# Optimization experiments

Measured on AMD Instinct MI355X. Metric: run time of the kernel, lower is better.

Reference implementation:

```python
import jax, jax.numpy as jnp
import numpy as np

B, V, H = 16384, 1024, 256


def setup_inputs() -> dict:
    key = jax.random.key(0)
    k1, k2 = jax.random.split(key)
    # binary spin configurations in {0,1}
    batch = jax.random.bernoulli(k1, 0.5, (B, V)).astype(jnp.float32)
    # small weights + negative hidden bias keep exp(log p*) finite in fp32
    weights_amp = jax.random.normal(k2, (H, V), dtype=jnp.float32) * (0.05 / np.sqrt(V))
    visible_bias_amp = jnp.zeros((V,), dtype=jnp.float32)
    hidden_bias_amp = -5.0 * jnp.ones((H,), dtype=jnp.float32)
    return {
        'batch': batch,
        'weights_amp': weights_amp,
        'visible_bias_amp': visible_bias_amp,
        'hidden_bias_amp': hidden_bias_amp,
        'k': 8,
    }


def _gibbs_sampling_amp(v0, W, vb, hb, k, key):
    """k steps of block Gibbs sampling, vectorized over the whole batch [B,V]."""
    keys = jax.random.split(key, 2 * k).reshape(k, 2)

    def step(v, ks):
        ph = jax.nn.sigmoid(v @ W.T + hb)                      # [B,H]
        h = (jax.random.uniform(ks[0], ph.shape) < ph).astype(v.dtype)
        pv = jax.nn.sigmoid(h @ W + vb)                        # [B,V]
        v = (jax.random.uniform(ks[1], pv.shape) < pv).astype(v.dtype)
        return v, None

    vk, _ = jax.lax.scan(step, v0, keys)
    return vk


def reference(batch, weights_amp, visible_bias_amp, hidden_bias_amp, k):
    W, vb, hb = weights_amp, visible_bias_amp, hidden_bias_amp
    nbatch = batch.shape[0]
    key = jax.random.key(42)

    vk = _gibbs_sampling_amp(batch, W, vb, hb, k, key)          # [B,V]

    ph0 = jax.nn.sigmoid(batch @ W.T + hb)                      # [B,H] positive-phase hidden probs
    pre_k = vk @ W.T + hb                                       # [B,H]
    phk = jax.nn.sigmoid(pre_k)                                 # [B,H] negative-phase hidden probs

    # unnormalized_probability_amp(vk) = exp(vk.vb + sum_j softplus((W vk + hb)_j))
    log_p = vk @ vb + jax.nn.softplus(pre_k).sum(axis=-1)       # [B]
    inv_norm = jnp.exp(-log_p) / nbatch                         # 1 / (len(batch) * p*(vk))

    # g_W = sum_b [outer(phk_b, vk_b) - outer(ph0_b, v0_b)] / norm_b
    g_w = (jnp.einsum('b,bh,bv->hv', inv_norm, phk, vk)
           - jnp.einsum('b,bh,bv->hv', inv_norm, ph0, batch))   # [H,V]
    g_vb = jnp.einsum('b,bv->v', inv_norm, vk - batch)          # [V]
    g_hb = jnp.einsum('b,bh->h', inv_norm, phk - ph0)           # [H]

    return jnp.concatenate([g_w.ravel(), g_vb, g_hb])
```

## Files before the change

### kernel.cpp

```cpp
#include <hip/hip_runtime.h>
#include <stdint.h>

#define B_DIM 16384
#define V_DIM 1024
#define H_DIM 256
#define K_STEPS 8

typedef short bf16x8 __attribute__((ext_vector_type(8)));
typedef float f32x4 __attribute__((ext_vector_type(4)));

__host__ __device__ inline uint32_t rotl32(uint32_t v, int r) {
#if defined(__HIP_DEVICE_COMPILE__)
    return __builtin_amdgcn_alignbit(v, v, (uint32_t)(32 - r));
#else
    return (v << r) | (v >> (32 - r));
#endif
}

__host__ __device__ inline void threefry2x32(uint32_t k0, uint32_t k1,
                                             uint32_t x0, uint32_t x1,
                                             uint32_t* o0, uint32_t* o1) {
    uint32_t k2 = k0 ^ k1 ^ 0x1BD11BDAu;
    x0 += k0; x1 += k1;
#define TF_RND(r) { x0 += x1; x1 = rotl32(x1, (r)); x1 ^= x0; }
    TF_RND(13) TF_RND(15) TF_RND(26) TF_RND(6)
    x0 += k1; x1 += k2 + 1u;
    TF_RND(17) TF_RND(29) TF_RND(16) TF_RND(24)
    x0 += k2; x1 += k0 + 2u;
    TF_RND(13) TF_RND(15) TF_RND(26) TF_RND(6)
    x0 += k0; x1 += k1 + 3u;
    TF_RND(17) TF_RND(29) TF_RND(16) TF_RND(24)
    x0 += k1; x1 += k2 + 4u;
    TF_RND(13) TF_RND(15) TF_RND(26) TF_RND(6)
    x0 += k2; x1 += k0 + 5u;
#undef TF_RND
    *o0 = x0; *o1 = x1;
}

__device__ inline float tf_uniform(uint32_t key0, uint32_t key1, uint32_t e) {
    uint32_t o0, o1;
    threefry2x32(key0, key1, 0u, e, &o0, &o1);
    uint32_t bits = o0 ^ o1;
    return __uint_as_float((bits >> 9) | 0x3f800000u) - 1.0f;
}

__device__ inline uint16_t bf16_rn(float f) {
    uint32_t u = __float_as_uint(f);
    uint32_t r = u + 0x7FFFu + ((u >> 16) & 1u);
    return (uint16_t)(r >> 16);
}
__device__ inline float bf16_to_f32(uint16_t h) {
    return __uint_as_float(((uint32_t)h) << 16);
}

__device__ inline void gload_lds16(const void* g, void* l) {
    __builtin_amdgcn_global_load_lds((const __attribute__((address_space(1))) uint32_t*)g,
                                     (__attribute__((address_space(3))) uint32_t*)l, 16, 0, 0);
}

template <int MODE>
__global__ __launch_bounds__(256, 4) void mfma_gemm(
    const ushort* __restrict__ A, const ushort* __restrict__ Bhi,
    const ushort* __restrict__ Blo, const float* __restrict__ bias,
    ushort* __restrict__ out, ushort* __restrict__ out2,
    int N, int K, uint32_t key0, uint32_t key1) {
    __shared__ __align__(16) ushort As[2][64 * 32];
    __shared__ __align__(16) ushort Bs[2][64 * 32];
    __shared__ __align__(16) ushort Bs2[2][64 * 32];

    const int tid = threadIdx.x;
    const int lane = tid & 63;
    const int w = tid >> 6;
    const int m0 = blockIdx.x * 64;
    const int n0 = blockIdx.y * 64;

    f32x4 acc[2][2] = {};

    const int wm = (w & 1) * 32;
    const int wn = (w >> 1) * 32;
    const int q = lane >> 4;
    const int l15 = lane & 15;
    const int srow = lane >> 2;
    const int scol = (lane & 3) * 8;

    const size_t arow = (size_t)(m0 + w * 16 + srow) * K;
    const size_t brow = (size_t)(n0 + w * 16 + srow) * K;

    for (int k0 = 0; k0 < K; k0 += 64) {
#pragma unroll
        for (int s = 0; s < 2; ++s) {
            gload_lds16(&A[arow + k0 + s * 32 + scol], &As[s][w * 512]);
            gload_lds16(&Bhi[brow + k0 + s * 32 + scol], &Bs[s][w * 512]);
            gload_lds16(&Blo[brow + k0 + s * 32 + scol], &Bs2[s][w * 512]);
        }
        __syncthreads();
#pragma unroll
        for (int s = 0; s < 2; ++s) {
            bf16x8 af[2], bh[2], bl[2];
#pragma unroll
            for (int i = 0; i < 2; ++i)
                af[i] = *(const bf16x8*)&As[s][(wm + i * 16 + l15) * 32 + q * 8];
#pragma unroll
            for (int j = 0; j < 2; ++j) {
                bh[j] = *(const bf16x8*)&Bs[s][(wn + j * 16 + l15) * 32 + q * 8];
                bl[j] = *(const bf16x8*)&Bs2[s][(wn + j * 16 + l15) * 32 + q * 8];
            }
#pragma unroll
            for (int i = 0; i < 2; ++i)
#pragma unroll
                for (int j = 0; j < 2; ++j) {
                    acc[i][j] = __builtin_amdgcn_mfma_f32_16x16x32_bf16(af[i], bh[j], acc[i][j], 0, 0, 0);
                    acc[i][j] = __builtin_amdgcn_mfma_f32_16x16x32_bf16(af[i], bl[j], acc[i][j], 0, 0, 0);
                }
        }
        __syncthreads();
    }

    const int orow = q * 4;
#pragma unroll
    for (int i = 0; i < 2; ++i) {
#pragma unroll
        for (int j = 0; j < 2; ++j) {
            int col = n0 + wn + j * 16 + l15;
            float bv = bias[col];
#pragma unroll
            for (int r = 0; r < 4; ++r) {
                int row = m0 + wm + i * 16 + orow + r;
                float val = acc[i][j][r] + bv;
                if (MODE == 0) {
                    float E = expf(-val);
                    uint32_t e = (uint32_t)row * (uint32_t)N + (uint32_t)col;
                    float u = tf_uniform(key0, key1, e);
                    out[(size_t)row * N + col] = (fmaf(u, E, u) < 1.0f) ? (ushort)0x3F80 : (ushort)0;
                } else if (MODE == 3) {
                    float E = expf(-val);
                    float sg = 1.0f / (1.0f + E);
                    uint32_t e = (uint32_t)row * (uint32_t)N + (uint32_t)col;
                    float u = tf_uniform(key0, key1, e);
                    out[(size_t)row * N + col] = (fmaf(u, E, u) < 1.0f) ? (ushort)0x3F80 : (ushort)0;
                    out2[(size_t)row * N + col] = bf16_rn(sg);
                } else {
                    float sg = 1.0f / (1.0f + expf(-val));
                    out[(size_t)row * N + col] = bf16_rn(sg);
                }
            }
        }
    }
}

__global__ __launch_bounds__(256, 8) void vsample_kernel(
    const ushort* __restrict__ h,
    const float* __restrict__ W,
    const float* __restrict__ vb,
    ushort* __restrict__ vout,
    uint32_t key0, uint32_t key1) {
    const int lane = threadIdx.x & 63;
    const int wid = threadIdx.x >> 6;

    float vbr[16];
#pragma unroll
    for (int t = 0; t < 16; ++t) vbr[t] = vb[lane + 64 * t];

    const int row_base = blockIdx.x * 8 + wid * 2;
#pragma unroll
    for (int rr = 0; rr < 2; ++rr) {
        const int b = row_base + rr;
        ushort4 hv = ((const ushort4*)(h + (size_t)b * H_DIM))[lane];
        unsigned long long masks[4];
        masks[0] = __ballot(hv.x != 0);
        masks[1] = __ballot(hv.y != 0);
        masks[2] = __ballot(hv.z != 0);
        masks[3] = __ballot(hv.w != 0);

        float acc[16];
#pragma unroll
        for (int t = 0; t < 16; ++t) acc[t] = 0.0f;

#pragma unroll
        for (int s = 0; s < 4; ++s) {
            unsigned long long m = masks[s];
            while (m) {
                int l = __ffsll(m) - 1;
                m &= m - 1;
                int j = l * 4 + s;
                const float* wrow = W + (size_t)j * V_DIM + lane;
#pragma unroll
                for (int t = 0; t < 16; ++t) acc[t] += wrow[64 * t];
            }
        }

        const uint32_t ebase = (uint32_t)b * (uint32_t)V_DIM + (uint32_t)lane;
        ushort* orow = vout + (size_t)b * V_DIM + lane;
#pragma unroll
        for (int t = 0; t < 16; ++t) {
            float pre = acc[t] + vbr[t];
            float E = expf(-pre);
            float u = tf_uniform(key0, key1, ebase + 64u * (uint32_t)t);
            orow[64 * t] = (fmaf(u, E, u) < 1.0f) ? (ushort)0x3F80 : (ushort)0;
        }
    }
}

__global__ __launch_bounds__(256, 4) void mfma_gemm_acc(
    const ushort* __restrict__ A, const ushort* __restrict__ Bt,
    float* __restrict__ out, int N, int K, int k_slice) {
    __shared__ __align__(16) ushort As[64 * 32];
    __shared__ __align__(16) ushort Bs[64 * 32];

    const int tid = threadIdx.x;
    const int lane = tid & 63;
    const int w = tid >> 6;
    const int m0 = blockIdx.x * 64;
    const int n0 = blockIdx.y * 64;
    const int kbase = blockIdx.z * k_slice;

    f32x4 acc[2][2] = {};

    const int wm = (w & 1) * 32;
    const int wn = (w >> 1) * 32;
    const int q = lane >> 4;
    const int l15 = lane & 15;
    const int srow = lane >> 2;
    const int scol = (lane & 3) * 8;

    const size_t arow = (size_t)(m0 + w * 16 + srow) * K;
    const size_t brow = (size_t)(n0 + w * 16 + srow) * K;

    for (int kt = 0; kt < k_slice; kt += 32) {
        const int k0 = kbase + kt;
        gload_lds16(&A[arow + k0 + scol], &As[w * 512]);
        gload_lds16(&Bt[brow + k0 + scol], &Bs[w * 512]);
        __syncthreads();
        bf16x8 af[2], bf[2];
#pragma unroll
        for (int i = 0; i < 2; ++i) {
            af[i] = *(const bf16x8*)&As[(wm + i * 16 + l15) * 32 + q * 8];
            bf[i] = *(const bf16x8*)&Bs[(wn + i * 16 + l15) * 32 + q * 8];
        }
#pragma unroll
        for (int i = 0; i < 2; ++i)
#pragma unroll
            for (int j = 0; j < 2; ++j)
                acc[i][j] = __builtin_amdgcn_mfma_f32_16x16x32_bf16(af[i], bf[j], acc[i][j], 0, 0, 0);
        __syncthreads();
    }

    const int orow = q * 4;
#pragma unroll
    for (int i = 0; i < 2; ++i)
#pragma unroll
        for (int j = 0; j < 2; ++j) {
            int col = n0 + wn + j * 16 + l15;
#pragma unroll
            for (int r = 0; r < 4; ++r) {
                int row = m0 + wm + i * 16 + orow + r;
                atomicAdd(&out[(size_t)row * N + col], acc[i][j][r]);
            }
        }
}

__global__ void wsplit_kernel(const float* __restrict__ W, ushort* __restrict__ whi,
                              ushort* __restrict__ wlo) {
    int idx = blockIdx.x * 256 + threadIdx.x;
    float w = W[idx];
    ushort hi = bf16_rn(w);
    float fhi = bf16_to_f32(hi);
    ushort lo = bf16_rn(w - fhi);
    whi[idx] = hi; wlo[idx] = lo;
}

__global__ void tobf16_kernel(const float* __restrict__ src, ushort* __restrict__ dst) {
    int idx = blockIdx.x * 256 + threadIdx.x;
    float4 f = ((const float4*)src)[idx];
    ushort4 o;
    o.x = bf16_rn(f.x); o.y = bf16_rn(f.y); o.z = bf16_rn(f.z); o.w = bf16_rn(f.w);
    ((ushort4*)dst)[idx] = o;
}

__global__ __launch_bounds__(256) void lognorm_kernel(
    const ushort* __restrict__ phk, const ushort* __restrict__ vk,
    const float* __restrict__ vb, float* __restrict__ inv) {
    int b = blockIdx.x;
    int tid = threadIdx.x;
    float p = bf16_to_f32(phk[(size_t)b * H_DIM + tid]);
    float s = -log1pf(-p);
    for (int j = tid; j < V_DIM; j += 256)
        s += bf16_to_f32(vk[(size_t)b * V_DIM + j]) * vb[j];
    for (int off = 32; off > 0; off >>= 1) s += __shfl_down(s, off, 64);
    __shared__ float wsum[4];
    int lane = tid & 63, wid = tid >> 6;
    if (lane == 0) wsum[wid] = s;
    __syncthreads();
    if (tid == 0) {
        float t = wsum[0] + wsum[1] + wsum[2] + wsum[3];
        inv[b] = expf(-t) * (1.0f / 16384.0f);
    }
}

__global__ void build_At(const ushort* __restrict__ P, const float* __restrict__ inv,
                         float sgn, ushort* __restrict__ At) {
    __shared__ float T[64][65];
    int c = threadIdx.x & 63;
    int rb = threadIdx.x >> 6;
    int b0 = blockIdx.x * 64;
    int h0 = blockIdx.y * 64;
    for (int r = rb; r < 64; r += 4) {
        int b = b0 + r;
        T[c][r] = sgn * inv[b] * bf16_to_f32(P[(size_t)b * H_DIM + h0 + c]);
    }
    __syncthreads();
    for (int r = rb; r < 64; r += 4)
        At[(size_t)(h0 + r) * B_DIM + b0 + c] = bf16_rn(T[r][c]);
}

__global__ void build_Bt(const ushort* __restrict__ Sb, const float* __restrict__ Sf,
                         int use_f32, ushort* __restrict__ Bt) {
    __shared__ ushort T[64][65];
    int c = threadIdx.x & 63;
    int rb = threadIdx.x >> 6;
    int b0 = blockIdx.x * 64;
    int v0 = blockIdx.y * 64;
    for (int r = rb; r < 64; r += 4) {
        int b = b0 + r;
        T[c][r] = use_f32 ? bf16_rn(Sf[(size_t)b * V_DIM + v0 + c])
                          : Sb[(size_t)b * V_DIM + v0 + c];
    }
    __syncthreads();
    for (int r = rb; r < 64; r += 4)
        Bt[(size_t)(v0 + r) * B_DIM + b0 + c] = T[r][c];
}

__global__ void gvb_kernel(const ushort* __restrict__ vk, const ushort* __restrict__ vbat,
                           const float* __restrict__ inv, float* __restrict__ gvb) {
    int col = blockIdx.x * 256 + threadIdx.x;
    int b0 = blockIdx.y * 512;
    float acc = 0.0f;
    for (int r = 0; r < 512; ++r) {
        int b = b0 + r;
        acc += inv[b] * (bf16_to_f32(vk[(size_t)b * V_DIM + col]) -
                         bf16_to_f32(vbat[(size_t)b * V_DIM + col]));
    }
    atomicAdd(&gvb[col], acc);
}

__global__ void ghb_kernel(const ushort* __restrict__ phk, const ushort* __restrict__ ph0,
                           const float* __restrict__ inv, float* __restrict__ ghb) {
    int col = threadIdx.x;
    int b0 = blockIdx.x * 256;
    float acc = 0.0f;
    for (int r = 0; r < 256; ++r) {
        int b = b0 + r;
        acc += inv[b] * (bf16_to_f32(phk[(size_t)b * H_DIM + col]) -
                         bf16_to_f32(ph0[(size_t)b * H_DIM + col]));
    }
    atomicAdd(&ghb[col], acc);
}

extern "C" void kernel_launch(void* const* d_in, const int* in_sizes, int n_in,
                              void* d_out, int out_size, void* d_ws, size_t ws_size,
                              hipStream_t stream) {
    const float* batch = (const float*)d_in[0];
    const float* W = (const float*)d_in[1];
    const float* vb = (const float*)d_in[2];
    const float* hb = (const float*)d_in[3];

    char* base = (char*)d_ws;
    ushort* w_hi  = (ushort*)(base + 0);
    ushort* w_lo  = (ushort*)(base + 524288);
    ushort* v_cur = (ushort*)(base + 2097152);
    float*  inv   = (float*)(base + 35651584);
    ushort* h_cur = (ushort*)(base + 35717120);
    ushort* At    = h_cur;
    ushort* batch_bf = (ushort*)(base + 44105728);
    ushort* Bt    = batch_bf;
    ushort* ph0b  = (ushort*)(base + 77660160);
    ushort* phkb  = (ushort*)(base + 86048768);

    float* gw  = (float*)d_out;
    float* gvb = gw + (size_t)H_DIM * V_DIM;
    float* ghb = gvb + V_DIM;

    hipMemsetAsync(d_out, 0, (size_t)out_size * sizeof(float), stream);

    uint32_t sk0[16], sk1[16];
    for (int n = 0; n < 16; ++n) threefry2x32(0u, 42u, 0u, (uint32_t)n, &sk0[n], &sk1[n]);

    wsplit_kernel<<<dim3(1024), dim3(256), 0, stream>>>(W, w_hi, w_lo);
    tobf16_kernel<<<dim3(B_DIM * V_DIM / 4 / 256), dim3(256), 0, stream>>>(batch, batch_bf);

    for (int i = 0; i < K_STEPS; ++i) {
        const ushort* vin = (i == 0) ? batch_bf : v_cur;
        if (i == 0) {
            mfma_gemm<3><<<dim3(B_DIM / 64, H_DIM / 64), dim3(256), 0, stream>>>(
                vin, w_hi, w_lo, hb, h_cur, ph0b, H_DIM, V_DIM, sk0[0], sk1[0]);
        } else {
            mfma_gemm<0><<<dim3(B_DIM / 64, H_DIM / 64), dim3(256), 0, stream>>>(
                vin, w_hi, w_lo, hb, h_cur, nullptr, H_DIM, V_DIM, sk0[2 * i], sk1[2 * i]);
        }
        vsample_kernel<<<dim3(B_DIM / 8), dim3(256), 0, stream>>>(
            h_cur, W, vb, v_cur, sk0[2 * i + 1], sk1[2 * i + 1]);
    }
    mfma_gemm<1><<<dim3(B_DIM / 64, H_DIM / 64), dim3(256), 0, stream>>>(
        v_cur, w_hi, w_lo, hb, phkb, nullptr, H_DIM, V_DIM, 0u, 0u);

    lognorm_kernel<<<dim3(B_DIM), dim3(256), 0, stream>>>(phkb, v_cur, vb, inv);
    ghb_kernel<<<dim3(B_DIM / 256), dim3(256), 0, stream>>>(phkb, ph0b, inv, ghb);
    gvb_kernel<<<dim3(V_DIM / 256, B_DIM / 512), dim3(256), 0, stream>>>(v_cur, batch_bf, inv, gvb);

    build_At<<<dim3(B_DIM / 64, H_DIM / 64), dim3(256), 0, stream>>>(phkb, inv, 1.0f, At);
    build_Bt<<<dim3(B_DIM / 64, V_DIM / 64), dim3(256), 0, stream>>>(v_cur, nullptr, 0, Bt);
    mfma_gemm_acc<<<dim3(H_DIM / 64, V_DIM / 64, 16), dim3(256), 0, stream>>>(
        At, Bt, gw, V_DIM, B_DIM, 1024);
    build_At<<<dim3(B_DIM / 64, H_DIM / 64), dim3(256), 0, stream>>>(ph0b, inv, -1.0f, At);
    build_Bt<<<dim3(B_DIM / 64, V_DIM / 64), dim3(256), 0, stream>>>(nullptr, batch, 1, Bt);
    mfma_gemm_acc<<<dim3(H_DIM / 64, V_DIM / 64, 16), dim3(256), 0, stream>>>(
        At, Bt, gw, V_DIM, B_DIM, 1024);
}
```

Before: 901.2 us.

## Fuse all Gibbs steps into one persistent per-row-tile kernel with LDS hidden state

Replaces the 17 separate launches of the hidden GEMM and visible sampling kernels with a single kernel. Each 512-thread block owns 32 batch rows and iterates all Gibbs steps plus the final phk computation. The sampled hidden units stay in LDS instead of round-tripping through global memory, and launch overhead between steps goes away. In exchange, each block streams the full 256-row split weight matrix every step, the grid shrinks to 512 blocks with a larger LDS footprint per block, and the GEMM tile becomes 32x256, which may reduce occupancy and latency hiding.

```diff
diff --git a/kernel.cpp b/kernel.cpp
--- a/kernel.cpp
+++ b/kernel.cpp
@@ -58,146 +58,143 @@
                                      (__attribute__((address_space(3))) uint32_t*)l, 16, 0, 0);
 }
 
-template <int MODE>
-__global__ __launch_bounds__(256, 4) void mfma_gemm(
-    const ushort* __restrict__ A, const ushort* __restrict__ Bhi,
-    const ushort* __restrict__ Blo, const float* __restrict__ bias,
-    ushort* __restrict__ out, ushort* __restrict__ out2,
-    int N, int K, uint32_t key0, uint32_t key1) {
-    __shared__ __align__(16) ushort As[2][64 * 32];
-    __shared__ __align__(16) ushort Bs[2][64 * 32];
-    __shared__ __align__(16) ushort Bs2[2][64 * 32];
+struct KeyPack { uint32_t hk0[8], hk1[8], vk0[8], vk1[8]; };
+
+__global__ __launch_bounds__(512, 4) void gibbs_fused(
+    const ushort* __restrict__ batch_bf,
+    const ushort* __restrict__ Whi, const ushort* __restrict__ Wlo,
+    const float* __restrict__ Wf, const float* __restrict__ vb,
+    const float* __restrict__ hb, ushort* __restrict__ v_cur,
+    ushort* __restrict__ ph0b, ushort* __restrict__ phkb, KeyPack kp) {
+    __shared__ __align__(16) ushort As[2][32 * 32];
+    __shared__ __align__(16) ushort BhS[2][256 * 32];
+    __shared__ __align__(16) ushort BlS[2][256 * 32];
 
     const int tid = threadIdx.x;
     const int lane = tid & 63;
     const int w = tid >> 6;
-    const int m0 = blockIdx.x * 64;
-    const int n0 = blockIdx.y * 64;
-
-    f32x4 acc[2][2] = {};
-
-    const int wm = (w & 1) * 32;
-    const int wn = (w >> 1) * 32;
+    const int m0 = blockIdx.x * 32;
+
+    const int wm = (w & 1) * 16;
+    const int wn = (w >> 1) * 64;
     const int q = lane >> 4;
     const int l15 = lane & 15;
     const int srow = lane >> 2;
     const int scol = (lane & 3) * 8;
 
-    const size_t arow = (size_t)(m0 + w * 16 + srow) * K;
-    const size_t brow = (size_t)(n0 + w * 16 + srow) * K;
-
-    for (int k0 = 0; k0 < K; k0 += 64) {
-#pragma unroll
-        for (int s = 0; s < 2; ++s) {
-            gload_lds16(&A[arow + k0 + s * 32 + scol], &As[s][w * 512]);
-            gload_lds16(&Bhi[brow + k0 + s * 32 + scol], &Bs[s][w * 512]);
-            gload_lds16(&Blo[brow + k0 + s * 32 + scol], &Bs2[s][w * 512]);
+    ushort* h_lds = &BhS[0][0];
+
+    for (int step = 0; step <= K_STEPS; ++step) {
+        const ushort* Asrc = (step == 0) ? batch_bf : v_cur;
+        f32x4 acc[4] = {};
+
+        for (int k0 = 0; k0 < V_DIM; k0 += 64) {
+            if (w < 4) {
+                const int s = w & 1, rh = w >> 1;
+                gload_lds16(&Asrc[(size_t)(m0 + rh * 16 + srow) * V_DIM + k0 + s * 32 + scol],
+                            &As[s][rh * 512]);
+            }
+#pragma unroll
+            for (int c = 0; c < 4; ++c) {
+                const int cc = w + 8 * c;
+                const int s = cc & 1, rb = cc >> 1;
+                const size_t off = (size_t)(rb * 16 + srow) * V_DIM + k0 + s * 32 + scol;
+                gload_lds16(&Whi[off], &BhS[s][rb * 512]);
+                gload_lds16(&Wlo[off], &BlS[s][rb * 512]);
+            }
+            __syncthreads();
+#pragma unroll
+            for (int s = 0; s < 2; ++s) {
+                bf16x8 af = *(const bf16x8*)&As[s][(wm + l15) * 32 + q * 8];
+#pragma unroll
+                for (int j = 0; j < 4; ++j) {
+                    bf16x8 bh = *(const bf16x8*)&BhS[s][(wn + j * 16 + l15) * 32 + q * 8];
+                    bf16x8 bl = *(const bf16x8*)&BlS[s][(wn + j * 16 + l15) * 32 + q * 8];
+                    acc[j] = __builtin_amdgcn_mfma_f32_16x16x32_bf16(af, bh, acc[j], 0, 0, 0);
+                    acc[j] = __builtin_amdgcn_mfma_f32_16x16x32_bf16(af, bl, acc[j], 0, 0, 0);
+                }
+            }
+            __syncthreads();
+        }
+
+        if (step == K_STEPS) {
+#pragma unroll
+            for (int j = 0; j < 4; ++j) {
+                const int col = wn + j * 16 + l15;
+                const float hbv = hb[col];
+#pragma unroll
+                for (int r = 0; r < 4; ++r) {
+                    const int row = m0 + wm + q * 4 + r;
+                    float val = acc[j][r] + hbv;
+                    phkb[(size_t)row * H_DIM + col] = bf16_rn(1.0f / (1.0f + expf(-val)));
+                }
+            }
+            break;
+        }
+
+        const uint32_t kh0 = kp.hk0[step], kh1 = kp.hk1[step];
+#pragma unroll
+        for (int j = 0; j < 4; ++j) {
+            const int col = wn + j * 16 + l15;
+            const float hbv = hb[col];
+#pragma unroll
+            for (int r = 0; r < 4; ++r) {
+                const int rowl = wm + q * 4 + r;
+                const int row = m0 + rowl;
+                float val = acc[j][r] + hbv;
+                float E = expf(-val);
+                float u = tf_uniform(kh0, kh1, (uint32_t)row * (uint32_t)H_DIM + (uint32_t)col);
+                h_lds[rowl * H_DIM + col] = (fmaf(u, E, u) < 1.0f) ? (ushort)0x3F80 : (ushort)0;
+                if (step == 0) {
+                    ph0b[(size_t)row * H_DIM + col] = bf16_rn(1.0f / (1.0f + E));
+                }
+            }
         }
         __syncthreads();
-#pragma unroll
-        for (int s = 0; s < 2; ++s) {
-            bf16x8 af[2], bh[2], bl[2];
-#pragma unroll
-            for (int i = 0; i < 2; ++i)
-                af[i] = *(const bf16x8*)&As[s][(wm + i * 16 + l15) * 32 + q * 8];
-#pragma unroll
-            for (int j = 0; j < 2; ++j) {
-                bh[j] = *(const bf16x8*)&Bs[s][(wn + j * 16 + l15) * 32 + q * 8];
-                bl[j] = *(const bf16x8*)&Bs2[s][(wn + j * 16 + l15) * 32 + q * 8];
-            }
-#pragma unroll
-            for (int i = 0; i < 2; ++i)
-#pragma unroll
-                for (int j = 0; j < 2; ++j) {
-                    acc[i][j] = __builtin_amdgcn_mfma_f32_16x16x32_bf16(af[i], bh[j], acc[i][j], 0, 0, 0);
-                    acc[i][j] = __builtin_amdgcn_mfma_f32_16x16x32_bf16(af[i], bl[j], acc[i][j], 0, 0, 0);
+
+        const uint32_t kv0 = kp.vk0[step], kv1 = kp.vk1[step];
+        float vbr[16];
+#pragma unroll
+        for (int t = 0; t < 16; ++t) vbr[t] = vb[lane + 64 * t];
+#pragma unroll
+        for (int rr = 0; rr < 4; ++rr) {
+            const int bl_ = w * 4 + rr;
+            const int b = m0 + bl_;
+            ushort4 hv = ((const ushort4*)(h_lds + bl_ * H_DIM))[lane];
+            unsigned long long masks[4];
+            masks[0] = __ballot(hv.x != 0);
+            masks[1] = __ballot(hv.y != 0);
+            masks[2] = __ballot(hv.z != 0);
+            masks[3] = __ballot(hv.w != 0);
+
+            float acc2[16];
+#pragma unroll
+            for (int t = 0; t < 16; ++t) acc2[t] = 0.0f;
+
+#pragma unroll
+            for (int s = 0; s < 4; ++s) {
+                unsigned long long m = masks[s];
+                while (m) {
+                    int l = __ffsll(m) - 1;
+                    m &= m - 1;
+                    int jj = l * 4 + s;
+                    const float* wrow = Wf + (size_t)jj * V_DIM + lane;
+#pragma unroll
+                    for (int t = 0; t < 16; ++t) acc2[t] += wrow[64 * t];
                 }
+            }
+
+            const uint32_t ebase = (uint32_t)b * (uint32_t)V_DIM + (uint32_t)lane;
+            ushort* orow = v_cur + (size_t)b * V_DIM + lane;
+#pragma unroll
+            for (int t = 0; t < 16; ++t) {
+                float pre = acc2[t] + vbr[t];
+                float E = expf(-pre);
+                float u = tf_uniform(kv0, kv1, ebase + 64u * (uint32_t)t);
+                orow[64 * t] = (fmaf(u, E, u) < 1.0f) ? (ushort)0x3F80 : (ushort)0;
+            }
         }
         __syncthreads();
-    }
-
-    const int orow = q * 4;
-#pragma unroll
-    for (int i = 0; i < 2; ++i) {
-#pragma unroll
-        for (int j = 0; j < 2; ++j) {
-            int col = n0 + wn + j * 16 + l15;
-            float bv = bias[col];
-#pragma unroll
-            for (int r = 0; r < 4; ++r) {
-                int row = m0 + wm + i * 16 + orow + r;
-                float val = acc[i][j][r] + bv;
-                if (MODE == 0) {
-                    float E = expf(-val);
-                    uint32_t e = (uint32_t)row * (uint32_t)N + (uint32_t)col;
-                    float u = tf_uniform(key0, key1, e);
-                    out[(size_t)row * N + col] = (fmaf(u, E, u) < 1.0f) ? (ushort)0x3F80 : (ushort)0;
-                } else if (MODE == 3) {
-                    float E = expf(-val);
-                    float sg = 1.0f / (1.0f + E);
-                    uint32_t e = (uint32_t)row * (uint32_t)N + (uint32_t)col;
-                    float u = tf_uniform(key0, key1, e);
-                    out[(size_t)row * N + col] = (fmaf(u, E, u) < 1.0f) ? (ushort)0x3F80 : (ushort)0;
-                    out2[(size_t)row * N + col] = bf16_rn(sg);
-                } else {
-                    float sg = 1.0f / (1.0f + expf(-val));
-                    out[(size_t)row * N + col] = bf16_rn(sg);
-                }
-            }
-        }
-    }
-}
-
-__global__ __launch_bounds__(256, 8) void vsample_kernel(
-    const ushort* __restrict__ h,
-    const float* __restrict__ W,
-    const float* __restrict__ vb,
-    ushort* __restrict__ vout,
-    uint32_t key0, uint32_t key1) {
-    const int lane = threadIdx.x & 63;
-    const int wid = threadIdx.x >> 6;
-
-    float vbr[16];
-#pragma unroll
-    for (int t = 0; t < 16; ++t) vbr[t] = vb[lane + 64 * t];
-
-    const int row_base = blockIdx.x * 8 + wid * 2;
-#pragma unroll
-    for (int rr = 0; rr < 2; ++rr) {
-        const int b = row_base + rr;
-        ushort4 hv = ((const ushort4*)(h + (size_t)b * H_DIM))[lane];
-        unsigned long long masks[4];
-        masks[0] = __ballot(hv.x != 0);
-        masks[1] = __ballot(hv.y != 0);
-        masks[2] = __ballot(hv.z != 0);
-        masks[3] = __ballot(hv.w != 0);
-
-        float acc[16];
-#pragma unroll
-        for (int t = 0; t < 16; ++t) acc[t] = 0.0f;
-
-#pragma unroll
-        for (int s = 0; s < 4; ++s) {
-            unsigned long long m = masks[s];
-            while (m) {
-                int l = __ffsll(m) - 1;
-                m &= m - 1;
-                int j = l * 4 + s;
-                const float* wrow = W + (size_t)j * V_DIM + lane;
-#pragma unroll
-                for (int t = 0; t < 16; ++t) acc[t] += wrow[64 * t];
-            }
-        }
-
-        const uint32_t ebase = (uint32_t)b * (uint32_t)V_DIM + (uint32_t)lane;
-        ushort* orow = vout + (size_t)b * V_DIM + lane;
-#pragma unroll
-        for (int t = 0; t < 16; ++t) {
-            float pre = acc[t] + vbr[t];
-            float E = expf(-pre);
-            float u = tf_uniform(key0, key1, ebase + 64u * (uint32_t)t);
-            orow[64 * t] = (fmaf(u, E, u) < 1.0f) ? (ushort)0x3F80 : (ushort)0;
-        }
     }
 }
 
@@ -369,8 +366,7 @@
     ushort* w_lo  = (ushort*)(base + 524288);
     ushort* v_cur = (ushort*)(base + 2097152);
     float*  inv   = (float*)(base + 35651584);
-    ushort* h_cur = (ushort*)(base + 35717120);
-    ushort* At    = h_cur;
+    ushort* At    = (ushort*)(base + 35717120);
     ushort* batch_bf = (ushort*)(base + 44105728);
     ushort* Bt    = batch_bf;
     ushort* ph0b  = (ushort*)(base + 77660160);
@@ -382,26 +378,17 @@
 
     hipMemsetAsync(d_out, 0, (size_t)out_size * sizeof(float), stream);
 
-    uint32_t sk0[16], sk1[16];
-    for (int n = 0; n < 16; ++n) threefry2x32(0u, 42u, 0u, (uint32_t)n, &sk0[n], &sk1[n]);
+    KeyPack kp;
+    for (int i = 0; i < K_STEPS; ++i) {
+        threefry2x32(0u, 42u, 0u, (uint32_t)(2 * i),     &kp.hk0[i], &kp.hk1[i]);
+        threefry2x32(0u, 42u, 0u, (uint32_t)(2 * i + 1), &kp.vk0[i], &kp.vk1[i]);
+    }
 
     wsplit_kernel<<<dim3(1024), dim3(256), 0, stream>>>(W, w_hi, w_lo);
     tobf16_kernel<<<dim3(B_DIM * V_DIM / 4 / 256), dim3(256), 0, stream>>>(batch, batch_bf);
 
-    for (int i = 0; i < K_STEPS; ++i) {
-        const ushort* vin = (i == 0) ? batch_bf : v_cur;
-        if (i == 0) {
-            mfma_gemm<3><<<dim3(B_DIM / 64, H_DIM / 64), dim3(256), 0, stream>>>(
-                vin, w_hi, w_lo, hb, h_cur, ph0b, H_DIM, V_DIM, sk0[0], sk1[0]);
-        } else {
-            mfma_gemm<0><<<dim3(B_DIM / 64, H_DIM / 64), dim3(256), 0, stream>>>(
-                vin, w_hi, w_lo, hb, h_cur, nullptr, H_DIM, V_DIM, sk0[2 * i], sk1[2 * i]);
-        }
-        vsample_kernel<<<dim3(B_DIM / 8), dim3(256), 0, stream>>>(
-            h_cur, W, vb, v_cur, sk0[2 * i + 1], sk1[2 * i + 1]);
-    }
-    mfma_gemm<1><<<dim3(B_DIM / 64, H_DIM / 64), dim3(256), 0, stream>>>(
-        v_cur, w_hi, w_lo, hb, phkb, nullptr, H_DIM, V_DIM, 0u, 0u);
+    gibbs_fused<<<dim3(B_DIM / 32), dim3(512), 0, stream>>>(
+        batch_bf, w_hi, w_lo, W, vb, hb, v_cur, ph0b, phkb, kp);
 
     lognorm_kernel<<<dim3(B_DIM), dim3(256), 0, stream>>>(phkb, v_cur, vb, inv);
     ghb_kernel<<<dim3(B_DIM / 256), dim3(256), 0, stream>>>(phkb, ph0b, inv, ghb);
```

Result: no change. 917.2 us (+1.8%).

## Overlap Gibbs GEMM and v-sampling across batch halves with swizzled LDS tiles

Applied to the files above, without the earlier changes.

Splits the batch into two halves and launches hybrid kernels in which some blocks run the v-sampling for one half while the others run the hidden GEMM for the other half. This staggers the Gibbs chain so the bandwidth-bound sampling and the MFMA-bound GEMM share the GPU in each launch. The GEMM and the accumulation GEMM also stage 64-wide K tiles into XOR-swizzled LDS layouts, with hi and lo weights interleaved in one buffer, to reduce bank conflicts and barrier count. The price is more complex scheduling, uneven block workloads inside a single grid, and reliance on careful half-to-half data dependencies between launches.

```diff
diff --git a/kernel.cpp b/kernel.cpp
--- a/kernel.cpp
+++ b/kernel.cpp
@@ -5,6 +5,7 @@
 #define V_DIM 1024
 #define H_DIM 256
 #define K_STEPS 8
+#define HALF_B 8192
 
 typedef short bf16x8 __attribute__((ext_vector_type(8)));
 typedef float f32x4 __attribute__((ext_vector_type(4)));
@@ -59,51 +60,64 @@
 }
 
 template <int MODE>
-__global__ __launch_bounds__(256, 4) void mfma_gemm(
+__device__ __forceinline__ void gemm_block(
+    const int m0, const int n0,
     const ushort* __restrict__ A, const ushort* __restrict__ Bhi,
     const ushort* __restrict__ Blo, const float* __restrict__ bias,
     ushort* __restrict__ out, ushort* __restrict__ out2,
-    int N, int K, uint32_t key0, uint32_t key1) {
-    __shared__ __align__(16) ushort As[2][64 * 32];
-    __shared__ __align__(16) ushort Bs[2][64 * 32];
-    __shared__ __align__(16) ushort Bs2[2][64 * 32];
-
+    const int N, const int K, const uint32_t key0, const uint32_t key1,
+    ushort* Am, ushort* Bm) {
     const int tid = threadIdx.x;
     const int lane = tid & 63;
     const int w = tid >> 6;
-    const int m0 = blockIdx.x * 64;
-    const int n0 = blockIdx.y * 64;
-
-    f32x4 acc[2][2] = {};
-
     const int wm = (w & 1) * 32;
     const int wn = (w >> 1) * 32;
     const int q = lane >> 4;
     const int l15 = lane & 15;
-    const int srow = lane >> 2;
-    const int scol = (lane & 3) * 8;
-
-    const size_t arow = (size_t)(m0 + w * 16 + srow) * K;
-    const size_t brow = (size_t)(n0 + w * 16 + srow) * K;
+
+    const ushort* asrc[2];
+#pragma unroll
+    for (int i = 0; i < 2; ++i) {
+        const int j = w * 2 + i;
+        const int row = j * 8 + (lane >> 3);
+        const int sl = (lane & 7) ^ (row & 7);
+        asrc[i] = A + (size_t)(m0 + row) * K + (sl >> 2) * 32 + (sl & 3) * 8;
+    }
+    const ushort* bsrc[4];
+#pragma unroll
+    for (int i = 0; i < 4; ++i) {
+        const int j = w * 4 + i;
+        const int row = j * 4 + (lane >> 4);
+        const int sl = (lane & 15) ^ (row & 15);
+        const int hl = (sl >> 2) & 1;
+        bsrc[i] = (hl ? Blo : Bhi) + (size_t)(n0 + row) * K + (sl >> 3) * 32 + (sl & 3) * 8;
+    }
+
+    f32x4 acc[2][2] = {};
 
     for (int k0 = 0; k0 < K; k0 += 64) {
 #pragma unroll
-        for (int s = 0; s < 2; ++s) {
-            gload_lds16(&A[arow + k0 + s * 32 + scol], &As[s][w * 512]);
-            gload_lds16(&Bhi[brow + k0 + s * 32 + scol], &Bs[s][w * 512]);
-            gload_lds16(&Blo[brow + k0 + s * 32 + scol], &Bs2[s][w * 512]);
-        }
+        for (int i = 0; i < 2; ++i)
+            gload_lds16(asrc[i] + k0, &Am[(w * 2 + i) * 512]);
+#pragma unroll
+        for (int i = 0; i < 4; ++i)
+            gload_lds16(bsrc[i] + k0, &Bm[(w * 4 + i) * 512]);
         __syncthreads();
 #pragma unroll
         for (int s = 0; s < 2; ++s) {
             bf16x8 af[2], bh[2], bl[2];
 #pragma unroll
-            for (int i = 0; i < 2; ++i)
-                af[i] = *(const bf16x8*)&As[s][(wm + i * 16 + l15) * 32 + q * 8];
+            for (int i = 0; i < 2; ++i) {
+                const int ra = wm + i * 16 + l15;
+                af[i] = *(const bf16x8*)((const char*)Am + ra * 128 +
+                                         (((s * 4 + q) ^ (ra & 7)) * 16));
+            }
 #pragma unroll
             for (int j = 0; j < 2; ++j) {
-                bh[j] = *(const bf16x8*)&Bs[s][(wn + j * 16 + l15) * 32 + q * 8];
-                bl[j] = *(const bf16x8*)&Bs2[s][(wn + j * 16 + l15) * 32 + q * 8];
+                const int rb = wn + j * 16 + l15;
+                const char* bb = (const char*)Bm + rb * 256;
+                bh[j] = *(const bf16x8*)(bb + (((s * 8 + q) ^ (rb & 15)) * 16));
+                bl[j] = *(const bf16x8*)(bb + (((s * 8 + 4 + q) ^ (rb & 15)) * 16));
             }
 #pragma unroll
             for (int i = 0; i < 2; ++i)
@@ -148,12 +162,10 @@
     }
 }
 
-__global__ __launch_bounds__(256, 8) void vsample_kernel(
-    const ushort* __restrict__ h,
-    const float* __restrict__ W,
-    const float* __restrict__ vb,
-    ushort* __restrict__ vout,
-    uint32_t key0, uint32_t key1) {
+__device__ __forceinline__ void vsample_block(
+    const ushort* __restrict__ h, const float* __restrict__ W,
+    const float* __restrict__ vb, ushort* __restrict__ vout,
+    uint32_t key0, uint32_t key1, int row_base) {
     const int lane = threadIdx.x & 63;
     const int wid = threadIdx.x >> 6;
 
@@ -161,10 +173,10 @@
 #pragma unroll
     for (int t = 0; t < 16; ++t) vbr[t] = vb[lane + 64 * t];
 
-    const int row_base = blockIdx.x * 8 + wid * 2;
+    const int rb2 = row_base + wid * 2;
 #pragma unroll
     for (int rr = 0; rr < 2; ++rr) {
-        const int b = row_base + rr;
+        const int b = rb2 + rr;
         ushort4 hv = ((const ushort4*)(h + (size_t)b * H_DIM))[lane];
         unsigned long long masks[4];
         masks[0] = __ballot(hv.x != 0);
@@ -201,11 +213,46 @@
     }
 }
 
+template <int MODE>
+__global__ __launch_bounds__(256, 4) void gemm_only(
+    const ushort* __restrict__ A, const ushort* __restrict__ Bhi,
+    const ushort* __restrict__ Blo, const float* __restrict__ bias,
+    ushort* __restrict__ out, ushort* __restrict__ out2,
+    uint32_t key0, uint32_t key1, int mbase) {
+    __shared__ __align__(16) ushort Am[64 * 64];
+    __shared__ __align__(16) ushort Bm[64 * 128];
+    gemm_block<MODE>(mbase + blockIdx.x * 64, blockIdx.y * 64, A, Bhi, Blo, bias,
+                     out, out2, H_DIM, V_DIM, key0, key1, Am, Bm);
+}
+
+template <int MODE>
+__global__ __launch_bounds__(256, 4) void hybrid_step(
+    const ushort* __restrict__ vin, const ushort* __restrict__ Whi,
+    const ushort* __restrict__ Wlo, const float* __restrict__ hb,
+    ushort* __restrict__ hout, ushort* __restrict__ out2,
+    uint32_t gk0, uint32_t gk1, int gemm_mbase,
+    const ushort* __restrict__ hprev, const float* __restrict__ Wf,
+    const float* __restrict__ vb, ushort* __restrict__ vout,
+    uint32_t vk0, uint32_t vk1, int vs_base, int nb_vs) {
+    __shared__ __align__(16) ushort Am[64 * 64];
+    __shared__ __align__(16) ushort Bm[64 * 128];
+    const int bid = blockIdx.x;
+    if (bid < nb_vs) {
+        vsample_block(hprev, Wf, vb, vout, vk0, vk1, vs_base + bid * 8);
+    } else {
+        const int g = bid - nb_vs;
+        const int gx = g & 127;
+        const int gy = g >> 7;
+        gemm_block<MODE>(gemm_mbase + gx * 64, gy * 64, vin, Whi, Wlo, hb,
+                         hout, out2, H_DIM, V_DIM, gk0, gk1, Am, Bm);
+    }
+}
+
 __global__ __launch_bounds__(256, 4) void mfma_gemm_acc(
     const ushort* __restrict__ A, const ushort* __restrict__ Bt,
     float* __restrict__ out, int N, int K, int k_slice) {
-    __shared__ __align__(16) ushort As[64 * 32];
-    __shared__ __align__(16) ushort Bs[64 * 32];
+    __shared__ __align__(16) ushort As[64 * 64];
+    __shared__ __align__(16) ushort Bs[64 * 64];
 
     const int tid = threadIdx.x;
     const int lane = tid & 63;
@@ -214,34 +261,51 @@
     const int n0 = blockIdx.y * 64;
     const int kbase = blockIdx.z * k_slice;
 
-    f32x4 acc[2][2] = {};
-
     const int wm = (w & 1) * 32;
     const int wn = (w >> 1) * 32;
     const int q = lane >> 4;
     const int l15 = lane & 15;
-    const int srow = lane >> 2;
-    const int scol = (lane & 3) * 8;
-
-    const size_t arow = (size_t)(m0 + w * 16 + srow) * K;
-    const size_t brow = (size_t)(n0 + w * 16 + srow) * K;
-
-    for (int kt = 0; kt < k_slice; kt += 32) {
+
+    const ushort* asrc[2];
+    const ushort* bsrc[2];
+#pragma unroll
+    for (int i = 0; i < 2; ++i) {
+        const int j = w * 2 + i;
+        const int row = j * 8 + (lane >> 3);
+        const int sl = (lane & 7) ^ (row & 7);
+        const size_t off = (size_t)row * K + (sl >> 2) * 32 + (sl & 3) * 8;
+        asrc[i] = A + (size_t)m0 * K + off;
+        bsrc[i] = Bt + (size_t)n0 * K + off;
+    }
+
+    f32x4 acc[2][2] = {};
+
+    for (int kt = 0; kt < k_slice; kt += 64) {
         const int k0 = kbase + kt;
-        gload_lds16(&A[arow + k0 + scol], &As[w * 512]);
-        gload_lds16(&Bt[brow + k0 + scol], &Bs[w * 512]);
+#pragma unroll
+        for (int i = 0; i < 2; ++i) {
+            gload_lds16(asrc[i] + k0, &As[(w * 2 + i) * 512]);
+            gload_lds16(bsrc[i] + k0, &Bs[(w * 2 + i) * 512]);
+        }
         __syncthreads();
-        bf16x8 af[2], bf[2];
-#pragma unroll
-        for (int i = 0; i < 2; ++i) {
-            af[i] = *(const bf16x8*)&As[(wm + i * 16 + l15) * 32 + q * 8];
-            bf[i] = *(const bf16x8*)&Bs[(wn + i * 16 + l15) * 32 + q * 8];
-        }
-#pragma unroll
-        for (int i = 0; i < 2; ++i)
-#pragma unroll
-            for (int j = 0; j < 2; ++j)
-                acc[i][j] = __builtin_amdgcn_mfma_f32_16x16x32_bf16(af[i], bf[j], acc[i][j], 0, 0, 0);
+#pragma unroll
+        for (int s = 0; s < 2; ++s) {
+            bf16x8 af[2], bf[2];
+#pragma unroll
+            for (int i = 0; i < 2; ++i) {
+                const int ra = wm + i * 16 + l15;
+                const int rb = wn + i * 16 + l15;
+                af[i] = *(const bf16x8*)((const char*)As + ra * 128 +
+                                         (((s * 4 + q) ^ (ra & 7)) * 16));
+                bf[i] = *(const bf16x8*)((const char*)Bs + rb * 128 +
+                                         (((s * 4 + q) ^ (rb & 7)) * 16));
+            }
+#pragma unroll
+            for (int i = 0; i < 2; ++i)
+#pragma unroll
+                for (int j = 0; j < 2; ++j)
+                    acc[i][j] = __builtin_amdgcn_mfma_f32_16x16x32_bf16(af[i], bf[j], acc[i][j], 0, 0, 0);
+        }
         __syncthreads();
     }
 
@@ -388,20 +452,36 @@
     wsplit_kernel<<<dim3(1024), dim3(256), 0, stream>>>(W, w_hi, w_lo);
     tobf16_kernel<<<dim3(B_DIM * V_DIM / 4 / 256), dim3(256), 0, stream>>>(batch, batch_bf);
 
-    for (int i = 0; i < K_STEPS; ++i) {
-        const ushort* vin = (i == 0) ? batch_bf : v_cur;
-        if (i == 0) {
-            mfma_gemm<3><<<dim3(B_DIM / 64, H_DIM / 64), dim3(256), 0, stream>>>(
-                vin, w_hi, w_lo, hb, h_cur, ph0b, H_DIM, V_DIM, sk0[0], sk1[0]);
+    const int NB_VS = HALF_B / 8;
+    const int NB_G  = (HALF_B / 64) * 4;
+    const dim3 HYB(NB_VS + NB_G);
+
+    gemm_only<3><<<dim3(128, 4), dim3(256), 0, stream>>>(
+        batch_bf, w_hi, w_lo, hb, h_cur, ph0b, sk0[0], sk1[0], 0);
+
+    for (int s = 0; s < K_STEPS; ++s) {
+        const ushort* vin = (s == 0) ? batch_bf : v_cur;
+        if (s == 0) {
+            hybrid_step<3><<<HYB, dim3(256), 0, stream>>>(
+                vin, w_hi, w_lo, hb, h_cur, ph0b, sk0[0], sk1[0], HALF_B,
+                h_cur, W, vb, v_cur, sk0[1], sk1[1], 0, NB_VS);
         } else {
-            mfma_gemm<0><<<dim3(B_DIM / 64, H_DIM / 64), dim3(256), 0, stream>>>(
-                vin, w_hi, w_lo, hb, h_cur, nullptr, H_DIM, V_DIM, sk0[2 * i], sk1[2 * i]);
-        }
-        vsample_kernel<<<dim3(B_DIM / 8), dim3(256), 0, stream>>>(
-            h_cur, W, vb, v_cur, sk0[2 * i + 1], sk1[2 * i + 1]);
-    }
-    mfma_gemm<1><<<dim3(B_DIM / 64, H_DIM / 64), dim3(256), 0, stream>>>(
-        v_cur, w_hi, w_lo, hb, phkb, nullptr, H_DIM, V_DIM, 0u, 0u);
+            hybrid_step<0><<<HYB, dim3(256), 0, stream>>>(
+                vin, w_hi, w_lo, hb, h_cur, nullptr, sk0[2 * s], sk1[2 * s], HALF_B,
+                h_cur, W, vb, v_cur, sk0[2 * s + 1], sk1[2 * s + 1], 0, NB_VS);
+        }
+        if (s < K_STEPS - 1) {
+            hybrid_step<0><<<HYB, dim3(256), 0, stream>>>(
+                v_cur, w_hi, w_lo, hb, h_cur, nullptr, sk0[2 * s + 2], sk1[2 * s + 2], 0,
+                h_cur, W, vb, v_cur, sk0[2 * s + 1], sk1[2 * s + 1], HALF_B, NB_VS);
+        } else {
+            hybrid_step<1><<<HYB, dim3(256), 0, stream>>>(
+                v_cur, w_hi, w_lo, hb, phkb, nullptr, 0u, 0u, 0,
+                h_cur, W, vb, v_cur, sk0[2 * s + 1], sk1[2 * s + 1], HALF_B, NB_VS);
+        }
+    }
+    gemm_only<1><<<dim3(128, 4), dim3(256), 0, stream>>>(
+        v_cur, w_hi, w_lo, hb, phkb, nullptr, 0u, 0u, HALF_B);
 
     lognorm_kernel<<<dim3(B_DIM), dim3(256), 0, stream>>>(phkb, v_cur, vb, inv);
     ghb_kernel<<<dim3(B_DIM / 256), dim3(256), 0, stream>>>(phkb, ph0b, inv, ghb);
```

Measured after the change: 859.2 us. 4.7% less time.
